# Optimization experiments

Measured on AMD Instinct MI355X. Metric: run time of the kernel, lower is better.

## Reference

```python
import jax, jax.numpy as jnp
import numpy as np

N_HEADS, D_MODEL, DK, DV = 16, 1024, 64, 64
B, S = 4, 2048


def setup_inputs() -> dict:
    key = jax.random.key(0)
    ks = jax.random.split(key, 7)
    scale = 1.0 / np.sqrt(D_MODEL)
    return {
        "Q": jax.random.normal(ks[0], (B, S, D_MODEL), dtype=jnp.float32),
        "K": jax.random.normal(ks[1], (B, S, D_MODEL), dtype=jnp.float32),
        "V": jax.random.normal(ks[2], (B, S, D_MODEL), dtype=jnp.float32),
        # Linear weights stored as [in, out] so y = x @ W (equivalent to torch x @ W.T)
        "w_q": jax.random.normal(ks[3], (D_MODEL, N_HEADS * DK), dtype=jnp.float32) * scale,
        "w_k": jax.random.normal(ks[4], (D_MODEL, N_HEADS * DK), dtype=jnp.float32) * scale,
        "w_v": jax.random.normal(ks[5], (D_MODEL, N_HEADS * DV), dtype=jnp.float32) * scale,
        "w_o": jax.random.normal(ks[6], (N_HEADS * DV, D_MODEL), dtype=jnp.float32) * scale,
    }


def reference(Q, K, V, w_q, w_k, w_v, w_o):
    b, s, _ = Q.shape
    # projections -> [B, H, S, d]
    q = (Q @ w_q).reshape(b, s, N_HEADS, DK).transpose(0, 2, 1, 3)
    k = (K @ w_k).reshape(b, s, N_HEADS, DK).transpose(0, 2, 1, 3)
    v = (V @ w_v).reshape(b, s, N_HEADS, DV).transpose(0, 2, 1, 3)
    # scaled dot-product attention, full [B,H,S,S] scores (matches source)
    scores = jnp.einsum("bhqd,bhkd->bhqk", q, k) / jnp.sqrt(jnp.float32(DK))
    attn = jax.nn.softmax(scores, axis=-1)
    x = jnp.einsum("bhqk,bhkd->bhqd", attn, v)
    x = x.transpose(0, 2, 1, 3).reshape(b, s, N_HEADS * DV)
    return x @ w_o
```

## Files before the change

kernel.cpp:

```cpp
#include <hip/hip_runtime.h>
#include <stdint.h>

#define B_   4
#define S_   2048
#define H_   16
#define D_   64
#define DM_  1024
#define NTOK (B_ * S_)

typedef __attribute__((ext_vector_type(8))) short short8;
typedef __attribute__((ext_vector_type(4))) float floatx4;

__device__ inline unsigned short f2bf(float f) {
  unsigned int u = __float_as_uint(f);
  u += 0x7FFFu + ((u >> 16) & 1u);
  return (unsigned short)(u >> 16);
}

__device__ inline floatx4 mfma_bf16(short8 a, short8 b, floatx4 c) {
  return __builtin_amdgcn_mfma_f32_16x16x32_bf16(a, b, c, 0, 0, 0);
}

__device__ inline unsigned int pack_bf2(float lo, float hi) {
  return __builtin_amdgcn_perm(__float_as_uint(hi), __float_as_uint(lo), 0x07060302u);
}

__device__ inline void gload_lds16(const unsigned short* g, unsigned short* l) {
  __builtin_amdgcn_global_load_lds(
      (const __attribute__((address_space(1))) unsigned int*)g,
      (__attribute__((address_space(3))) unsigned int*)l, 16, 0, 0);
}

__global__ __launch_bounds__(256) void cast_bf16_kernel(const float* __restrict__ in,
                                                        unsigned short* __restrict__ out,
                                                        int n4) {
  int i = blockIdx.x * 256 + threadIdx.x;
  if (i < n4) {
    float4 v = ((const float4*)in)[i];
    ushort4 o;
    o.x = f2bf(v.x); o.y = f2bf(v.y); o.z = f2bf(v.z); o.w = f2bf(v.w);
    ((ushort4*)out)[i] = o;
  }
}

__global__ __launch_bounds__(256) void wt_kernel(const float* __restrict__ w0,
                                                 const float* __restrict__ w1,
                                                 const float* __restrict__ w2,
                                                 const float* __restrict__ w3,
                                                 unsigned short* __restrict__ o0,
                                                 unsigned short* __restrict__ o1,
                                                 unsigned short* __restrict__ o2,
                                                 unsigned short* __restrict__ o3) {
  __shared__ unsigned short T[64 * 68];
  const float* w = blockIdx.z == 0 ? w0 : blockIdx.z == 1 ? w1 : blockIdx.z == 2 ? w2 : w3;
  unsigned short* o = blockIdx.z == 0 ? o0 : blockIdx.z == 1 ? o1 : blockIdx.z == 2 ? o2 : o3;
  const int tid = threadIdx.x;
  const int R0 = blockIdx.y * 64;
  const int C0 = blockIdx.x * 64;
  for (int it = 0; it < 16; it++) {
    int lr = it * 4 + (tid >> 6), lc = tid & 63;
    T[lc * 68 + lr] = f2bf(w[(size_t)(R0 + lr) * 1024 + C0 + lc]);
  }
  __syncthreads();
  for (int it = 0; it < 2; it++) {
    int orow = it * 32 + (tid >> 3), oc = (tid & 7) * 8;
    union { ushort4 h[2]; short8 v8; } u;
    u.h[0] = *(const ushort4*)(T + orow * 68 + oc);
    u.h[1] = *(const ushort4*)(T + orow * 68 + oc + 4);
    *(short8*)(o + (size_t)(C0 + orow) * 1024 + R0 + oc) = u.v8;
  }
}

template <int MODE>
__global__ __launch_bounds__(256) void gemm_bt_kernel(const unsigned short* __restrict__ A,
                                                      const unsigned short* __restrict__ BT,
                                                      void* __restrict__ Cout,
                                                      float scale) {
  constexpr int K = 1024;
  __shared__ unsigned short As[128 * 32];
  __shared__ unsigned short Bs[128 * 32];

  const int tid  = threadIdx.x;
  const int wave = tid >> 6, lane = tid & 63;
  const int quad = lane >> 4, l16 = lane & 15;
  const int wm = wave >> 1, wn = wave & 1;
  const int mb = blockIdx.x * 8 + (blockIdx.y >> 3);
  const int nb = blockIdx.y & 7;
  const int m0 = mb * 128, n0 = nb * 128;

  floatx4 acc[4][4] = {};

  for (int k0 = 0; k0 < K; k0 += 32) {
    for (int p = 0; p < 2; p++) {
      int i = p * 256 + wave * 64 + lane;
      int row = i >> 2, c = i & 3;
      gload_lds16(A  + (size_t)(m0 + row) * K + k0 + c * 8,
                  As + (size_t)(p * 256 + wave * 64) * 8);
      gload_lds16(BT + (size_t)(n0 + row) * K + k0 + c * 8,
                  Bs + (size_t)(p * 256 + wave * 64) * 8);
    }
    __syncthreads();

    short8 af[4], bfr[4];
    for (int f = 0; f < 4; f++) {
      af[f]  = *(const short8*)(As + (wm * 64 + f * 16 + l16) * 32 + quad * 8);
      bfr[f] = *(const short8*)(Bs + (wn * 64 + f * 16 + l16) * 32 + quad * 8);
    }
    for (int fm = 0; fm < 4; fm++)
      for (int fn = 0; fn < 4; fn++)
        acc[fm][fn] = mfma_bf16(af[fm], bfr[fn], acc[fm][fn]);
    __syncthreads();
  }

  for (int fm = 0; fm < 4; fm++)
    for (int fn = 0; fn < 4; fn++)
      for (int r = 0; r < 4; r++) {
        int gm = m0 + wm * 64 + fm * 16 + quad * 4 + r;
        int gn = n0 + wn * 64 + fn * 16 + l16;
        float val = acc[fm][fn][r] * scale;
        if (MODE == 0) {
          int b = gm >> 11, s = gm & 2047;
          int h = gn >> 6,  d = gn & 63;
          ((unsigned short*)Cout)[((size_t)((b * H_ + h) * S_ + s) << 6) + d] = f2bf(val);
        } else if (MODE == 1) {
          ((float*)Cout)[((size_t)gm << 10) + gn] = val;
        } else {
          int b = gm >> 11, s = gm & 2047;
          int h = gn >> 6,  d = gn & 63;
          int p = ((s & 63) >> 4) + (s & 15) * 4;
          ((unsigned short*)Cout)[(((size_t)(b * H_ + h) * 64 + d) << 11) + (s & ~63) + p] = f2bf(val);
        }
      }
}

__global__ __launch_bounds__(512, 4) void attn_kernel(const unsigned short* __restrict__ q,
                                                      const unsigned short* __restrict__ k,
                                                      const unsigned short* __restrict__ vT,
                                                      unsigned short* __restrict__ X) {
  __shared__ unsigned short Ks[2][64 * 64];
  __shared__ unsigned short Vt[2][64 * 64];
  __shared__ unsigned short Ps[8][16 * 72];

  const int tid  = threadIdx.x;
  const int wave = tid >> 6, lane = tid & 63;
  const int quad = lane >> 4, l16 = lane & 15;
  const int bh = blockIdx.x * 8 + (blockIdx.y >> 3);
  const int q0 = (blockIdx.y & 7) * 256;

  const unsigned short* qh = q  + (size_t)bh * S_ * 64;
  const unsigned short* kh = k  + (size_t)bh * S_ * 64;
  const unsigned short* vh = vT + (size_t)bh * 64 * S_;

  const int sr  = tid >> 3;
  const int sgc = (tid & 7) ^ (sr & 7);

  short8 qf[2][2];
  for (int qt = 0; qt < 2; qt++) {
    int row = q0 + wave * 32 + qt * 16 + l16;
    for (int kk = 0; kk < 2; kk++)
      qf[qt][kk] = *(const short8*)(qh + (size_t)row * 64 + kk * 32 + quad * 8);
  }

  short8 onesb = {};
  if (l16 == 0)
    for (int e = 0; e < 8; e++) onesb[e] = (short)0x3F80;

  const floatx4 fz = {};
  floatx4 O[2][4] = {};
  floatx4 lacc[2] = {};

  gload_lds16(kh + (size_t)sr * 64 + sgc * 8,       Ks[0] + (size_t)(wave * 64) * 8);
  gload_lds16(vh + (size_t)sr * S_ + 0 + sgc * 8,   Vt[0] + (size_t)(wave * 64) * 8);

  int cur = 0;
  for (int j0 = 0; j0 < S_; j0 += 64) {
    __syncthreads();

    if (j0 + 64 < S_) {
      int nxt = cur ^ 1;
      gload_lds16(kh + (size_t)(j0 + 64 + sr) * 64 + sgc * 8,
                  Ks[nxt] + (size_t)(wave * 64) * 8);
      gload_lds16(vh + (size_t)sr * S_ + (j0 + 64) + sgc * 8,
                  Vt[nxt] + (size_t)(wave * 64) * 8);
    }

    short8 kf[4][2];
    for (int jf = 0; jf < 4; jf++)
      for (int kk = 0; kk < 2; kk++) {
        int sl = (kk * 4 + quad) ^ (l16 & 7);
        kf[jf][kk] = *(const short8*)(Ks[cur] + (jf * 16 + l16) * 64 + sl * 8);
      }

    unsigned short* pw = Ps[wave];
    short8 pa[2][2];
    for (int qt = 0; qt < 2; qt++) {
      floatx4 s[4];
      for (int jf = 0; jf < 4; jf++) {
        s[jf] = mfma_bf16(qf[qt][0], kf[jf][0], fz);
        s[jf] = mfma_bf16(qf[qt][1], kf[jf][1], s[jf]);
      }
      for (int r = 0; r < 4; r++) {
        float e0 = __builtin_amdgcn_exp2f(s[0][r]);
        float e1 = __builtin_amdgcn_exp2f(s[1][r]);
        float e2 = __builtin_amdgcn_exp2f(s[2][r]);
        float e3 = __builtin_amdgcn_exp2f(s[3][r]);
        uint2 pk;
        pk.x = pack_bf2(e0, e1);
        pk.y = pack_bf2(e2, e3);
        *(uint2*)(pw + (quad * 4 + r) * 72 + l16 * 4) = pk;
      }
      pa[qt][0] = *(const short8*)(pw + l16 * 72 + quad * 8);
      pa[qt][1] = *(const short8*)(pw + l16 * 72 + 32 + quad * 8);
      lacc[qt] = mfma_bf16(pa[qt][0], onesb, lacc[qt]);
      lacc[qt] = mfma_bf16(pa[qt][1], onesb, lacc[qt]);
    }

    for (int df = 0; df < 4; df++) {
      int sl0 = quad ^ (l16 & 7);
      int sl1 = (4 + quad) ^ (l16 & 7);
      short8 v0 = *(const short8*)(Vt[cur] + (df * 16 + l16) * 64 + sl0 * 8);
      short8 v1 = *(const short8*)(Vt[cur] + (df * 16 + l16) * 64 + sl1 * 8);
      for (int qt = 0; qt < 2; qt++) {
        O[qt][df] = mfma_bf16(pa[qt][0], v0, O[qt][df]);
        O[qt][df] = mfma_bf16(pa[qt][1], v1, O[qt][df]);
      }
    }
    cur ^= 1;
  }

  const int b = bh >> 4, h = bh & 15;
  for (int qt = 0; qt < 2; qt++)
    for (int r = 0; r < 4; r++) {
      float lsum = __shfl(lacc[qt][r], (lane & 48));
      float inv = 1.0f / lsum;
      int row = q0 + wave * 32 + qt * 16 + quad * 4 + r;
      unsigned short* dst = X + ((size_t)(b * S_ + row) << 10) + h * 64;
      for (int df = 0; df < 4; df++)
        dst[df * 16 + l16] = f2bf(O[qt][df][r] * inv);
    }
}

extern "C" void kernel_launch(void* const* d_in, const int* in_sizes, int n_in,
                              void* d_out, int out_size, void* d_ws, size_t ws_size,
                              hipStream_t stream) {
  const float* Q  = (const float*)d_in[0];
  const float* K  = (const float*)d_in[1];
  const float* V  = (const float*)d_in[2];
  const float* wq = (const float*)d_in[3];
  const float* wk = (const float*)d_in[4];
  const float* wv = (const float*)d_in[5];
  const float* wo = (const float*)d_in[6];

  char* ws = (char*)d_ws;
  unsigned short* buf0 = (unsigned short*)ws;
  unsigned short* wqT  = (unsigned short*)(ws + (size_t)(16 << 20));
  unsigned short* wkT  = (unsigned short*)(ws + (size_t)(18 << 20));
  unsigned short* wvT  = (unsigned short*)(ws + (size_t)(20 << 20));
  unsigned short* woT  = (unsigned short*)(ws + (size_t)(22 << 20));
  unsigned short* qP   = (unsigned short*)(ws + (size_t)(24 << 20));
  unsigned short* kP   = (unsigned short*)(ws + (size_t)(40 << 20));
  unsigned short* vTg  = (unsigned short*)(ws + (size_t)(56 << 20));

  const int n4 = NTOK * DM_ / 4;
  const float SC = 0.18033688011112043f;

  wt_kernel<<<dim3(16, 16, 4), dim3(256), 0, stream>>>(wq, wk, wv, wo, wqT, wkT, wvT, woT);

  cast_bf16_kernel<<<dim3(8192), dim3(256), 0, stream>>>(Q, buf0, n4);
  gemm_bt_kernel<0><<<dim3(8, 64), dim3(256), 0, stream>>>(buf0, wqT, qP, SC);
  cast_bf16_kernel<<<dim3(8192), dim3(256), 0, stream>>>(K, buf0, n4);
  gemm_bt_kernel<0><<<dim3(8, 64), dim3(256), 0, stream>>>(buf0, wkT, kP, 1.0f);
  cast_bf16_kernel<<<dim3(8192), dim3(256), 0, stream>>>(V, buf0, n4);
  gemm_bt_kernel<2><<<dim3(8, 64), dim3(256), 0, stream>>>(buf0, wvT, vTg, 1.0f);

  attn_kernel<<<dim3(8, 64), dim3(512), 0, stream>>>(qP, kP, vTg, buf0);

  gemm_bt_kernel<1><<<dim3(8, 64), dim3(256), 0, stream>>>(buf0, woT, (float*)d_out, 1.0f);
}
```

Baseline: 340.7 us.

## Fuse fp32-to-bf16 cast into a single batched QKV projection kernel

Drops the three standalone cast kernels and replaces the three projection GEMM launches with one proj_kernel over blockIdx.z. It loads fp32 activations straight into LDS through global_load_lds and converts them to bf16 in registers with v_cvt_pk_bf16_f32 before the MFMA. The LDS layout also becomes k-chunk-major for both operands to change the bank access pattern. This removes the intermediate bf16 write and re-read of 3x32MB of activations and two launches, and puts all three projections in one grid. In exchange each block loads twice as many A bytes per K step and adds conversion instructions in the inner loop.

```diff
diff --git a/kernel.cpp b/kernel.cpp
--- a/kernel.cpp
+++ b/kernel.cpp
@@ -25,22 +25,16 @@
   return __builtin_amdgcn_perm(__float_as_uint(hi), __float_as_uint(lo), 0x07060302u);
 }
 
+__device__ inline unsigned int cvt_pk_bf16(float lo, float hi) {
+  unsigned int r;
+  asm("v_cvt_pk_bf16_f32 %0, %1, %2" : "=v"(r) : "v"(lo), "v"(hi));
+  return r;
+}
+
 __device__ inline void gload_lds16(const unsigned short* g, unsigned short* l) {
   __builtin_amdgcn_global_load_lds(
       (const __attribute__((address_space(1))) unsigned int*)g,
       (__attribute__((address_space(3))) unsigned int*)l, 16, 0, 0);
-}
-
-__global__ __launch_bounds__(256) void cast_bf16_kernel(const float* __restrict__ in,
-                                                        unsigned short* __restrict__ out,
-                                                        int n4) {
-  int i = blockIdx.x * 256 + threadIdx.x;
-  if (i < n4) {
-    float4 v = ((const float4*)in)[i];
-    ushort4 o;
-    o.x = f2bf(v.x); o.y = f2bf(v.y); o.z = f2bf(v.z); o.w = f2bf(v.w);
-    ((ushort4*)out)[i] = o;
-  }
 }
 
 __global__ __launch_bounds__(256) void wt_kernel(const float* __restrict__ w0,
@@ -71,14 +65,23 @@
   }
 }
 
-template <int MODE>
-__global__ __launch_bounds__(256) void gemm_bt_kernel(const unsigned short* __restrict__ A,
-                                                      const unsigned short* __restrict__ BT,
-                                                      void* __restrict__ Cout,
-                                                      float scale) {
+__global__ __launch_bounds__(256) void proj_kernel(
+    const float* __restrict__ Qf, const float* __restrict__ Kf,
+    const float* __restrict__ Vf,
+    const unsigned short* __restrict__ wqT, const unsigned short* __restrict__ wkT,
+    const unsigned short* __restrict__ wvT,
+    unsigned short* __restrict__ qP, unsigned short* __restrict__ kP,
+    unsigned short* __restrict__ vTg, float sc) {
   constexpr int K = 1024;
-  __shared__ unsigned short As[128 * 32];
-  __shared__ unsigned short Bs[128 * 32];
+  __shared__ __align__(16) float          As[8 * 128 * 4];
+  __shared__ __align__(16) unsigned short Bs[4 * 128 * 8];
+
+  const int z = blockIdx.z;
+  const float* A           = z == 0 ? Qf  : z == 1 ? Kf  : Vf;
+  const unsigned short* BT = z == 0 ? wqT : z == 1 ? wkT : wvT;
+  unsigned short* Cout     = z == 0 ? qP  : z == 1 ? kP  : vTg;
+  const float scale        = z == 0 ? sc : 1.0f;
+  const int mode           = (z == 2) ? 2 : 0;
 
   const int tid  = threadIdx.x;
   const int wave = tid >> 6, lane = tid & 63;
@@ -91,20 +94,91 @@
   floatx4 acc[4][4] = {};
 
   for (int k0 = 0; k0 < K; k0 += 32) {
+    for (int p = 0; p < 4; p++) {
+      int si = p * 256 + tid;
+      int r = si & 127, c = si >> 7;
+      gload_lds16((const unsigned short*)(A + (size_t)(m0 + r) * K + k0 + c * 4),
+                  (unsigned short*)As + (size_t)(p * 256 + wave * 64) * 8);
+    }
     for (int p = 0; p < 2; p++) {
-      int i = p * 256 + wave * 64 + lane;
-      int row = i >> 2, c = i & 3;
-      gload_lds16(A  + (size_t)(m0 + row) * K + k0 + c * 8,
-                  As + (size_t)(p * 256 + wave * 64) * 8);
-      gload_lds16(BT + (size_t)(n0 + row) * K + k0 + c * 8,
+      int si = p * 256 + tid;
+      int r = si & 127, c = si >> 7;
+      gload_lds16(BT + (size_t)(n0 + r) * K + k0 + c * 8,
                   Bs + (size_t)(p * 256 + wave * 64) * 8);
     }
     __syncthreads();
 
     short8 af[4], bfr[4];
     for (int f = 0; f < 4; f++) {
-      af[f]  = *(const short8*)(As + (wm * 64 + f * 16 + l16) * 32 + quad * 8);
-      bfr[f] = *(const short8*)(Bs + (wn * 64 + f * 16 + l16) * 32 + quad * 8);
+      int ra = wm * 64 + f * 16 + l16;
+      float4 a0 = *(const float4*)(As + (2 * quad) * 512 + ra * 4);
+      float4 a1 = *(const float4*)(As + (2 * quad + 1) * 512 + ra * 4);
+      union { unsigned int u[4]; short8 s8; } pk;
+      pk.u[0] = cvt_pk_bf16(a0.x, a0.y);
+      pk.u[1] = cvt_pk_bf16(a0.z, a0.w);
+      pk.u[2] = cvt_pk_bf16(a1.x, a1.y);
+      pk.u[3] = cvt_pk_bf16(a1.z, a1.w);
+      af[f] = pk.s8;
+      int rb = wn * 64 + f * 16 + l16;
+      bfr[f] = *(const short8*)(Bs + ((size_t)quad * 128 + rb) * 8);
+    }
+    for (int fm = 0; fm < 4; fm++)
+      for (int fn = 0; fn < 4; fn++)
+        acc[fm][fn] = mfma_bf16(af[fm], bfr[fn], acc[fm][fn]);
+    __syncthreads();
+  }
+
+  for (int fm = 0; fm < 4; fm++)
+    for (int fn = 0; fn < 4; fn++)
+      for (int r = 0; r < 4; r++) {
+        int gm = m0 + wm * 64 + fm * 16 + quad * 4 + r;
+        int gn = n0 + wn * 64 + fn * 16 + l16;
+        float val = acc[fm][fn][r] * scale;
+        int b = gm >> 11, s = gm & 2047;
+        int h = gn >> 6,  d = gn & 63;
+        if (mode == 0) {
+          Cout[((size_t)((b * H_ + h) * S_ + s) << 6) + d] = f2bf(val);
+        } else {
+          int p = ((s & 63) >> 4) + (s & 15) * 4;
+          Cout[(((size_t)(b * H_ + h) * 64 + d) << 11) + (s & ~63) + p] = f2bf(val);
+        }
+      }
+}
+
+template <int MODE>
+__global__ __launch_bounds__(256) void gemm_bt_kernel(const unsigned short* __restrict__ A,
+                                                      const unsigned short* __restrict__ BT,
+                                                      void* __restrict__ Cout,
+                                                      float scale) {
+  constexpr int K = 1024;
+  __shared__ __align__(16) unsigned short As[4 * 128 * 8];
+  __shared__ __align__(16) unsigned short Bs[4 * 128 * 8];
+
+  const int tid  = threadIdx.x;
+  const int wave = tid >> 6, lane = tid & 63;
+  const int quad = lane >> 4, l16 = lane & 15;
+  const int wm = wave >> 1, wn = wave & 1;
+  const int mb = blockIdx.x * 8 + (blockIdx.y >> 3);
+  const int nb = blockIdx.y & 7;
+  const int m0 = mb * 128, n0 = nb * 128;
+
+  floatx4 acc[4][4] = {};
+
+  for (int k0 = 0; k0 < K; k0 += 32) {
+    for (int p = 0; p < 2; p++) {
+      int si = p * 256 + tid;
+      int r = si & 127, c = si >> 7;
+      gload_lds16(A  + (size_t)(m0 + r) * K + k0 + c * 8,
+                  As + (size_t)(p * 256 + wave * 64) * 8);
+      gload_lds16(BT + (size_t)(n0 + r) * K + k0 + c * 8,
+                  Bs + (size_t)(p * 256 + wave * 64) * 8);
+    }
+    __syncthreads();
+
+    short8 af[4], bfr[4];
+    for (int f = 0; f < 4; f++) {
+      af[f]  = *(const short8*)(As + ((size_t)quad * 128 + wm * 64 + f * 16 + l16) * 8);
+      bfr[f] = *(const short8*)(Bs + ((size_t)quad * 128 + wn * 64 + f * 16 + l16) * 8);
     }
     for (int fm = 0; fm < 4; fm++)
       for (int fn = 0; fn < 4; fn++)
@@ -261,17 +335,12 @@
   unsigned short* kP   = (unsigned short*)(ws + (size_t)(40 << 20));
   unsigned short* vTg  = (unsigned short*)(ws + (size_t)(56 << 20));
 
-  const int n4 = NTOK * DM_ / 4;
   const float SC = 0.18033688011112043f;
 
   wt_kernel<<<dim3(16, 16, 4), dim3(256), 0, stream>>>(wq, wk, wv, wo, wqT, wkT, wvT, woT);
 
-  cast_bf16_kernel<<<dim3(8192), dim3(256), 0, stream>>>(Q, buf0, n4);
-  gemm_bt_kernel<0><<<dim3(8, 64), dim3(256), 0, stream>>>(buf0, wqT, qP, SC);
-  cast_bf16_kernel<<<dim3(8192), dim3(256), 0, stream>>>(K, buf0, n4);
-  gemm_bt_kernel<0><<<dim3(8, 64), dim3(256), 0, stream>>>(buf0, wkT, kP, 1.0f);
-  cast_bf16_kernel<<<dim3(8192), dim3(256), 0, stream>>>(V, buf0, n4);
-  gemm_bt_kernel<2><<<dim3(8, 64), dim3(256), 0, stream>>>(buf0, wvT, vTg, 1.0f);
+  proj_kernel<<<dim3(8, 64, 3), dim3(256), 0, stream>>>(Q, K, V, wqT, wkT, wvT,
+                                                        qP, kP, vTg, SC);
 
   attn_kernel<<<dim3(8, 64), dim3(512), 0, stream>>>(qP, kP, vTg, buf0);
 
```

Measured after the change: 447.7 us. +31.4%, slower.

## Batch QKV casts and projections into single launches with larger double-buffered GEMM tiles

Applied to the files above, without the earlier changes.

Three cast kernels become one grid-strided launch that writes bf16 copies of Q, K and V into separate buffers, reusing the output buffer as scratch. The three projection GEMMs become one launch indexed by blockIdx, using a new 256x128 tile kernel with 512 threads, a K-step of 64, XOR-swizzled LDS and double-buffered async global-to-LDS loads. The output projection uses the same kernel. This cuts launch count and serialization, improves operand reuse, and lets loads overlap with MFMA, at the cost of much more LDS (96KB), which may limit occupancy.

```diff
diff --git a/kernel.cpp b/kernel.cpp
--- a/kernel.cpp
+++ b/kernel.cpp
@@ -31,11 +31,16 @@
       (__attribute__((address_space(3))) unsigned int*)l, 16, 0, 0);
 }
 
-__global__ __launch_bounds__(256) void cast_bf16_kernel(const float* __restrict__ in,
-                                                        unsigned short* __restrict__ out,
-                                                        int n4) {
-  int i = blockIdx.x * 256 + threadIdx.x;
-  if (i < n4) {
+__global__ __launch_bounds__(256) void cast3_kernel(const float* __restrict__ Q,
+                                                    const float* __restrict__ Kf,
+                                                    const float* __restrict__ V,
+                                                    unsigned short* __restrict__ qB,
+                                                    unsigned short* __restrict__ kB,
+                                                    unsigned short* __restrict__ vB) {
+  const float* in = blockIdx.z == 0 ? Q : blockIdx.z == 1 ? Kf : V;
+  unsigned short* out = blockIdx.z == 0 ? qB : blockIdx.z == 1 ? kB : vB;
+  const int n4 = NTOK * DM_ / 4;
+  for (int i = blockIdx.x * 256 + threadIdx.x; i < n4; i += gridDim.x * 256) {
     float4 v = ((const float4*)in)[i];
     ushort4 o;
     o.x = f2bf(v.x); o.y = f2bf(v.y); o.z = f2bf(v.z); o.w = f2bf(v.w);
@@ -71,58 +76,102 @@
   }
 }
 
-template <int MODE>
-__global__ __launch_bounds__(256) void gemm_bt_kernel(const unsigned short* __restrict__ A,
-                                                      const unsigned short* __restrict__ BT,
-                                                      void* __restrict__ Cout,
-                                                      float scale) {
+__global__ __launch_bounds__(512) void gemm256_kernel(
+    const unsigned short* __restrict__ A0, const unsigned short* __restrict__ A1,
+    const unsigned short* __restrict__ A2,
+    const unsigned short* __restrict__ Bt0, const unsigned short* __restrict__ Bt1,
+    const unsigned short* __restrict__ Bt2,
+    void* __restrict__ C0, void* __restrict__ C1, void* __restrict__ C2,
+    int mode_z0, float scale_z0) {
   constexpr int K = 1024;
-  __shared__ unsigned short As[128 * 32];
-  __shared__ unsigned short Bs[128 * 32];
+  __shared__ __align__(16) unsigned short As[2][256 * 64];
+  __shared__ __align__(16) unsigned short Bs[2][128 * 64];
 
   const int tid  = threadIdx.x;
   const int wave = tid >> 6, lane = tid & 63;
   const int quad = lane >> 4, l16 = lane & 15;
-  const int wm = wave >> 1, wn = wave & 1;
-  const int mb = blockIdx.x * 8 + (blockIdx.y >> 3);
-  const int nb = blockIdx.y & 7;
-  const int m0 = mb * 128, n0 = nb * 128;
-
-  floatx4 acc[4][4] = {};
-
-  for (int k0 = 0; k0 < K; k0 += 32) {
-    for (int p = 0; p < 2; p++) {
-      int i = p * 256 + wave * 64 + lane;
-      int row = i >> 2, c = i & 3;
-      gload_lds16(A  + (size_t)(m0 + row) * K + k0 + c * 8,
-                  As + (size_t)(p * 256 + wave * 64) * 8);
-      gload_lds16(BT + (size_t)(n0 + row) * K + k0 + c * 8,
-                  Bs + (size_t)(p * 256 + wave * 64) * 8);
-    }
+  const int wm = wave >> 2, wn = wave & 3;
+
+  const int g  = blockIdx.x * gridDim.y + blockIdx.y;
+  const int z  = g >> 8;
+  const int rz = g & 255;
+  const int mb = rz >> 3, nb = rz & 7;
+  const int m0 = mb * 256, n0 = nb * 128;
+
+  const unsigned short* A  = z == 0 ? A0  : z == 1 ? A1  : A2;
+  const unsigned short* BT = z == 0 ? Bt0 : z == 1 ? Bt1 : Bt2;
+  void* Cout               = z == 0 ? C0  : z == 1 ? C1  : C2;
+  const int   mode  = z == 0 ? mode_z0 : (z == 2 ? 2 : 0);
+  const float scale = z == 0 ? scale_z0 : 1.0f;
+
+  floatx4 acc[8][2] = {};
+
+#define STAGE256(k0, buf)                                              \
+  do {                                                                 \
+    _Pragma("unroll")                                                  \
+    for (int p = 0; p < 4; p++) {                                      \
+      int si = p * 512 + tid;                                          \
+      int rr = si >> 3;                                                \
+      int gc = (si & 7) ^ (rr & 7);                                    \
+      gload_lds16(A + (size_t)(m0 + rr) * K + (k0) + gc * 8,           \
+                  As[buf] + (size_t)(p * 512 + wave * 64) * 8);        \
+    }                                                                  \
+    _Pragma("unroll")                                                  \
+    for (int p = 0; p < 2; p++) {                                      \
+      int si = p * 512 + tid;                                          \
+      int rr = si >> 3;                                                \
+      int gc = (si & 7) ^ (rr & 7);                                    \
+      gload_lds16(BT + (size_t)(n0 + rr) * K + (k0) + gc * 8,          \
+                  Bs[buf] + (size_t)(p * 512 + wave * 64) * 8);        \
+    }                                                                  \
+  } while (0)
+
+  STAGE256(0, 0);
+
+  int cur = 0;
+  for (int k0 = 0; k0 < K; k0 += 64) {
     __syncthreads();
 
-    short8 af[4], bfr[4];
-    for (int f = 0; f < 4; f++) {
-      af[f]  = *(const short8*)(As + (wm * 64 + f * 16 + l16) * 32 + quad * 8);
-      bfr[f] = *(const short8*)(Bs + (wn * 64 + f * 16 + l16) * 32 + quad * 8);
-    }
-    for (int fm = 0; fm < 4; fm++)
-      for (int fn = 0; fn < 4; fn++)
-        acc[fm][fn] = mfma_bf16(af[fm], bfr[fn], acc[fm][fn]);
-    __syncthreads();
-  }
-
-  for (int fm = 0; fm < 4; fm++)
-    for (int fn = 0; fn < 4; fn++)
+    if (k0 + 64 < K) STAGE256(k0 + 64, cur ^ 1);
+
+    short8 bfr[2][2];
+#pragma unroll
+    for (int n = 0; n < 2; n++)
+#pragma unroll
+      for (int kk = 0; kk < 2; kk++) {
+        int rb = wn * 32 + n * 16 + l16;
+        int j = kk * 4 + quad;
+        bfr[n][kk] = *(const short8*)(Bs[cur] + rb * 64 + (j ^ (rb & 7)) * 8);
+      }
+#pragma unroll
+    for (int f = 0; f < 8; f++) {
+      int ra = wm * 128 + f * 16 + l16;
+      short8 a0 = *(const short8*)(As[cur] + ra * 64 + ((quad)     ^ (ra & 7)) * 8);
+      short8 a1 = *(const short8*)(As[cur] + ra * 64 + ((4 + quad) ^ (ra & 7)) * 8);
+#pragma unroll
+      for (int n = 0; n < 2; n++) {
+        acc[f][n] = mfma_bf16(a0, bfr[n][0], acc[f][n]);
+        acc[f][n] = mfma_bf16(a1, bfr[n][1], acc[f][n]);
+      }
+    }
+    cur ^= 1;
+  }
+#undef STAGE256
+
+#pragma unroll
+  for (int f = 0; f < 8; f++)
+#pragma unroll
+    for (int n = 0; n < 2; n++)
+#pragma unroll
       for (int r = 0; r < 4; r++) {
-        int gm = m0 + wm * 64 + fm * 16 + quad * 4 + r;
-        int gn = n0 + wn * 64 + fn * 16 + l16;
-        float val = acc[fm][fn][r] * scale;
-        if (MODE == 0) {
+        int gm = m0 + wm * 128 + f * 16 + quad * 4 + r;
+        int gn = n0 + wn * 32 + n * 16 + l16;
+        float val = acc[f][n][r] * scale;
+        if (mode == 0) {
           int b = gm >> 11, s = gm & 2047;
           int h = gn >> 6,  d = gn & 63;
           ((unsigned short*)Cout)[((size_t)((b * H_ + h) * S_ + s) << 6) + d] = f2bf(val);
-        } else if (MODE == 1) {
+        } else if (mode == 1) {
           ((float*)Cout)[((size_t)gm << 10) + gn] = val;
         } else {
           int b = gm >> 11, s = gm & 2047;
@@ -261,19 +310,21 @@
   unsigned short* kP   = (unsigned short*)(ws + (size_t)(40 << 20));
   unsigned short* vTg  = (unsigned short*)(ws + (size_t)(56 << 20));
 
-  const int n4 = NTOK * DM_ / 4;
+  unsigned short* qB = (unsigned short*)d_out;
+  unsigned short* kB = qB + (size_t)8 * 1024 * 1024;
+  unsigned short* vB = buf0;
+
   const float SC = 0.18033688011112043f;
 
   wt_kernel<<<dim3(16, 16, 4), dim3(256), 0, stream>>>(wq, wk, wv, wo, wqT, wkT, wvT, woT);
 
-  cast_bf16_kernel<<<dim3(8192), dim3(256), 0, stream>>>(Q, buf0, n4);
-  gemm_bt_kernel<0><<<dim3(8, 64), dim3(256), 0, stream>>>(buf0, wqT, qP, SC);
-  cast_bf16_kernel<<<dim3(8192), dim3(256), 0, stream>>>(K, buf0, n4);
-  gemm_bt_kernel<0><<<dim3(8, 64), dim3(256), 0, stream>>>(buf0, wkT, kP, 1.0f);
-  cast_bf16_kernel<<<dim3(8192), dim3(256), 0, stream>>>(V, buf0, n4);
-  gemm_bt_kernel<2><<<dim3(8, 64), dim3(256), 0, stream>>>(buf0, wvT, vTg, 1.0f);
+  cast3_kernel<<<dim3(2048, 1, 3), dim3(256), 0, stream>>>(Q, K, V, qB, kB, vB);
+
+  gemm256_kernel<<<dim3(8, 96), dim3(512), 0, stream>>>(
+      qB, kB, vB, wqT, wkT, wvT, qP, kP, vTg, 0, SC);
 
   attn_kernel<<<dim3(8, 64), dim3(512), 0, stream>>>(qP, kP, vTg, buf0);
 
-  gemm_bt_kernel<1><<<dim3(8, 64), dim3(256), 0, stream>>>(buf0, woT, (float*)d_out, 1.0f);
-}
+  gemm256_kernel<<<dim3(8, 32), dim3(512), 0, stream>>>(
+      buf0, buf0, buf0, woT, woT, woT, d_out, d_out, d_out, 1, 1.0f);
+}
```

Result: slower. 357.7 us (+5.0%).
